# Kernel optimization log

Measured on AMD Instinct MI355X. Metric: run time of the kernel, lower is better.

The kernel has to match this reference:

```python
import jax, jax.numpy as jnp
import numpy as np

ALPHA = 0.5
EPS = 1e-6


def setup_inputs() -> dict:
    key = jax.random.key(0)
    k1, k2, k3 = jax.random.split(key, 3)
    B, N = 8192, 4096
    y_pred = jax.random.uniform(k1, (B, N), dtype=jnp.float32)
    y_true = jax.random.randint(k2, (B, N), 0, 2).astype(jnp.float32)
    depth_weights = jax.random.uniform(k3, (B, N), dtype=jnp.float32)
    return {"y_pred": y_pred, "y_true": y_true, "depth_weights": depth_weights}


def reference(y_pred, y_true, depth_weights):
    B, N = y_true.shape
    # --- weighted BCE ---
    bce = -(y_true * jnp.log(y_pred + EPS) + (1.0 - y_true) * jnp.log(1.0 - y_pred + EPS))
    wbce = jnp.mean(depth_weights * bce)

    # --- continuity-weighted loss: max run of correct predictions per row ---
    y_bin = (y_pred > 0.5).astype(y_true.dtype)
    correct = (y_bin == y_true)  # bool [B, N]
    idx = jnp.arange(N, dtype=jnp.int32)
    # position (1-based) of most recent incorrect element; 0 if none yet
    reset = jnp.where(correct, 0, idx + 1)  # [B, N]
    last_reset = jax.lax.cummax(reset, axis=1)  # [B, N]
    streak = (idx + 1)[None, :] - last_reset  # current run length at each position
    max_streak = jnp.max(streak, axis=1).astype(jnp.float32)  # [B]
    cwl = jnp.mean(1.0 - max_streak / N)

    return ALPHA * wbce + (1.0 - ALPHA) * cwl
```

## Files before the change

### kernel.cpp

```cpp
#include <hip/hip_runtime.h>

#define EPS 1e-6f

struct RunStats { int len, pre, suf, mx; };

__device__ inline RunStats rcombine(const RunStats& a, const RunStats& b) {
    RunStats r;
    r.len = a.len + b.len;
    r.pre = (a.pre == a.len) ? (a.len + b.pre) : a.pre;
    r.suf = (b.suf == b.len) ? (b.len + a.suf) : b.suf;
    r.mx  = max(max(a.mx, b.mx), a.suf + b.pre);
    return r;
}

__global__ __launch_bounds__(256) void row_kernel(
        const float* __restrict__ yp, const float* __restrict__ yt,
        const float* __restrict__ dw,
        float* __restrict__ row_wbce, int* __restrict__ row_streak) {
    const int row  = blockIdx.x;
    const int lane = threadIdx.x & 63;
    const int wave = threadIdx.x >> 6;
    const long base = (long)row * 4096;

    float sum = 0.0f;
    RunStats wstat = {0, 0, 0, 0};

    #pragma unroll
    for (int j = 0; j < 4; ++j) {
        const int e = wave * 1024 + j * 256 + lane * 4;
        const float4 p = *(const float4*)(yp + base + e);
        const float4 t = *(const float4*)(yt + base + e);
        const float4 w = *(const float4*)(dw + base + e);

        const float px[4] = {p.x, p.y, p.z, p.w};
        const float tx[4] = {t.x, t.y, t.z, t.w};
        const float wx[4] = {w.x, w.y, w.z, w.w};

        int bits = 0;
        #pragma unroll
        for (int c = 0; c < 4; ++c) {
            const float l1 = __logf(px[c] + EPS);
            const float l2 = __logf(1.0f - px[c] + EPS);
            const float bce = -(tx[c] * l1 + (1.0f - tx[c]) * l2);
            sum += wx[c] * bce;
            const bool pb = px[c] > 0.5f;
            const bool tb = tx[c] != 0.0f;
            bits |= (int)(pb == tb) << c;
        }

        int run = 0, m = 0;
        #pragma unroll
        for (int c = 0; c < 4; ++c) {
            run = ((bits >> c) & 1) ? run + 1 : 0;
            m = max(m, run);
        }
        const int pre = (bits & 1) ? ((bits & 2) ? ((bits & 4) ? ((bits & 8) ? 4 : 3) : 2) : 1) : 0;

        int packed = pre | (run << 10) | (m << 20);
        int alen = 4;
        #pragma unroll
        for (int off = 1; off < 64; off <<= 1) {
            const int o = __shfl_down(packed, off);
            const int apre = packed & 1023, asuf = (packed >> 10) & 1023, amx = packed >> 20;
            const int bpre = o & 1023,      bsuf = (o >> 10) & 1023,      bmx = o >> 20;
            const int npre = (apre == alen) ? (alen + bpre) : apre;
            const int nsuf = (bsuf == alen) ? (alen + asuf) : bsuf;
            const int nmx  = max(max(amx, bmx), asuf + bpre);
            packed = npre | (nsuf << 10) | (nmx << 20);
            alen <<= 1;
        }
        RunStats g;
        g.len = 256;
        g.pre = packed & 1023;
        g.suf = (packed >> 10) & 1023;
        g.mx  = packed >> 20;
        wstat = rcombine(wstat, g);
    }

    #pragma unroll
    for (int off = 32; off; off >>= 1) sum += __shfl_down(sum, off);

    __shared__ RunStats sstat[4];
    __shared__ float ssum[4];
    if (lane == 0) { sstat[wave] = wstat; ssum[wave] = sum; }
    __syncthreads();
    if (threadIdx.x == 0) {
        RunStats r = rcombine(rcombine(sstat[0], sstat[1]), rcombine(sstat[2], sstat[3]));
        row_wbce[row]   = ssum[0] + ssum[1] + ssum[2] + ssum[3];
        row_streak[row] = r.mx;
    }
}

__global__ __launch_bounds__(256) void finalize_kernel(
        const float* __restrict__ row_wbce, const int* __restrict__ row_streak,
        int rows, float* __restrict__ out) {
    double s = 0.0;
    long long st = 0;
    for (int i = threadIdx.x; i < rows; i += 256) {
        s  += (double)row_wbce[i];
        st += (long long)row_streak[i];
    }
    __shared__ double sd[256];
    __shared__ long long sl[256];
    sd[threadIdx.x] = s; sl[threadIdx.x] = st;
    __syncthreads();
    for (int o = 128; o; o >>= 1) {
        if (threadIdx.x < o) {
            sd[threadIdx.x] += sd[threadIdx.x + o];
            sl[threadIdx.x] += sl[threadIdx.x + o];
        }
        __syncthreads();
    }
    if (threadIdx.x == 0) {
        const double total = (double)rows * 4096.0;
        const double wbce = sd[0] / total;
        const double cwl  = 1.0 - (double)sl[0] / total;
        out[0] = (float)(0.5 * wbce + 0.5 * cwl);
    }
}

extern "C" void kernel_launch(void* const* d_in, const int* in_sizes, int n_in,
                              void* d_out, int out_size, void* d_ws, size_t ws_size,
                              hipStream_t stream) {
    const float* yp = (const float*)d_in[0];
    const float* yt = (const float*)d_in[1];
    const float* dw = (const float*)d_in[2];
    float* out = (float*)d_out;

    const int rows = in_sizes[0] / 4096;
    float* row_wbce  = (float*)d_ws;
    int*   row_streak = (int*)((char*)d_ws + (size_t)rows * sizeof(float));

    row_kernel<<<rows, 256, 0, stream>>>(yp, yt, dw, row_wbce, row_streak);
    finalize_kernel<<<1, 256, 0, stream>>>(row_wbce, row_streak, rows, out);
}
```

Before: 358.7 us.

## Give each thread 16 contiguous elements, use one log, bitmask run stats

Each thread now loads 16 contiguous elements (four float4 per input, all issued up front) instead of four strided float4 groups. BCE uses a single log per element by selecting p or 1-p from the binary label, with the negation moved to the end. Run statistics are computed from a 16-bit mask with ctz/clz and a shift-and loop, so only one cross-lane scan per wave is needed instead of four. The finalize kernel grows to 1024 threads. The single-log form assumes labels are exactly 0 or 1, and the denser load pattern may change coalescing.

Result: faster. 349.4 us (-2.6%).

```diff
diff --git a/kernel.cpp b/kernel.cpp
--- a/kernel.cpp
+++ b/kernel.cpp
@@ -20,91 +20,90 @@
     const int row  = blockIdx.x;
     const int lane = threadIdx.x & 63;
     const int wave = threadIdx.x >> 6;
-    const long base = (long)row * 4096;
+    const long base = (long)row * 4096 + wave * 1024 + lane * 16;
+
+    float4 p[4], t[4], w[4];
+    #pragma unroll
+    for (int q = 0; q < 4; ++q) {
+        p[q] = *(const float4*)(yp + base + q * 4);
+        t[q] = *(const float4*)(yt + base + q * 4);
+        w[q] = *(const float4*)(dw + base + q * 4);
+    }
 
     float sum = 0.0f;
-    RunStats wstat = {0, 0, 0, 0};
-
+    unsigned mask = 0;
     #pragma unroll
-    for (int j = 0; j < 4; ++j) {
-        const int e = wave * 1024 + j * 256 + lane * 4;
-        const float4 p = *(const float4*)(yp + base + e);
-        const float4 t = *(const float4*)(yt + base + e);
-        const float4 w = *(const float4*)(dw + base + e);
-
-        const float px[4] = {p.x, p.y, p.z, p.w};
-        const float tx[4] = {t.x, t.y, t.z, t.w};
-        const float wx[4] = {w.x, w.y, w.z, w.w};
-
-        int bits = 0;
+    for (int q = 0; q < 4; ++q) {
+        const float pp[4] = {p[q].x, p[q].y, p[q].z, p[q].w};
+        const float tt[4] = {t[q].x, t[q].y, t[q].z, t[q].w};
+        const float ww[4] = {w[q].x, w[q].y, w[q].z, w[q].w};
         #pragma unroll
         for (int c = 0; c < 4; ++c) {
-            const float l1 = __logf(px[c] + EPS);
-            const float l2 = __logf(1.0f - px[c] + EPS);
-            const float bce = -(tx[c] * l1 + (1.0f - tx[c]) * l2);
-            sum += wx[c] * bce;
-            const bool pb = px[c] > 0.5f;
-            const bool tb = tx[c] != 0.0f;
-            bits |= (int)(pb == tb) << c;
+            const bool tb = tt[c] != 0.0f;
+            const float v = (tb ? pp[c] : 1.0f - pp[c]) + EPS;
+            sum = fmaf(ww[c], __logf(v), sum);
+            const bool pb = pp[c] > 0.5f;
+            mask |= (unsigned)(pb == tb) << (q * 4 + c);
         }
+    }
 
-        int run = 0, m = 0;
-        #pragma unroll
-        for (int c = 0; c < 4; ++c) {
-            run = ((bits >> c) & 1) ? run + 1 : 0;
-            m = max(m, run);
-        }
-        const int pre = (bits & 1) ? ((bits & 2) ? ((bits & 4) ? ((bits & 8) ? 4 : 3) : 2) : 1) : 0;
-
-        int packed = pre | (run << 10) | (m << 20);
-        int alen = 4;
-        #pragma unroll
-        for (int off = 1; off < 64; off <<= 1) {
-            const int o = __shfl_down(packed, off);
-            const int apre = packed & 1023, asuf = (packed >> 10) & 1023, amx = packed >> 20;
-            const int bpre = o & 1023,      bsuf = (o >> 10) & 1023,      bmx = o >> 20;
-            const int npre = (apre == alen) ? (alen + bpre) : apre;
-            const int nsuf = (bsuf == alen) ? (alen + asuf) : bsuf;
-            const int nmx  = max(max(amx, bmx), asuf + bpre);
-            packed = npre | (nsuf << 10) | (nmx << 20);
-            alen <<= 1;
-        }
-        RunStats g;
-        g.len = 256;
-        g.pre = packed & 1023;
-        g.suf = (packed >> 10) & 1023;
-        g.mx  = packed >> 20;
-        wstat = rcombine(wstat, g);
-    }
+    int pre = __builtin_ctz(~mask);
+    int suf = __builtin_clz(~(mask << 16));
+    int mx = 0;
+    { unsigned x = mask; while (x) { x &= (x << 1); ++mx; } }
 
     #pragma unroll
     for (int off = 32; off; off >>= 1) sum += __shfl_down(sum, off);
 
+    int packed = pre | (suf << 10) | (mx << 20);
+    int alen = 16;
+    #pragma unroll
+    for (int off = 1; off < 32; off <<= 1) {
+        const int o = __shfl_down(packed, off);
+        const int apre = packed & 1023, asuf = (packed >> 10) & 1023, amx = packed >> 20;
+        const int bpre = o & 1023,      bsuf = (o >> 10) & 1023,      bmx = o >> 20;
+        const int npre = (apre == alen) ? (alen + bpre) : apre;
+        const int nsuf = (bsuf == alen) ? (alen + asuf) : bsuf;
+        const int nmx  = max(max(amx, bmx), asuf + bpre);
+        packed = npre | (nsuf << 10) | (nmx << 20);
+        alen <<= 1;
+    }
+    RunStats g;
+    {
+        const int o = __shfl_down(packed, 32);
+        const int apre = packed & 1023, asuf = (packed >> 10) & 1023, amx = packed >> 20;
+        const int bpre = o & 1023,      bsuf = (o >> 10) & 1023,      bmx = o >> 20;
+        g.len = 1024;
+        g.pre = (apre == 512) ? (512 + bpre) : apre;
+        g.suf = (bsuf == 512) ? (512 + asuf) : bsuf;
+        g.mx  = max(max(amx, bmx), asuf + bpre);
+    }
+
     __shared__ RunStats sstat[4];
     __shared__ float ssum[4];
-    if (lane == 0) { sstat[wave] = wstat; ssum[wave] = sum; }
+    if (lane == 0) { sstat[wave] = g; ssum[wave] = sum; }
     __syncthreads();
     if (threadIdx.x == 0) {
         RunStats r = rcombine(rcombine(sstat[0], sstat[1]), rcombine(sstat[2], sstat[3]));
-        row_wbce[row]   = ssum[0] + ssum[1] + ssum[2] + ssum[3];
+        row_wbce[row]   = -(ssum[0] + ssum[1] + ssum[2] + ssum[3]);
         row_streak[row] = r.mx;
     }
 }
 
-__global__ __launch_bounds__(256) void finalize_kernel(
+__global__ __launch_bounds__(1024) void finalize_kernel(
         const float* __restrict__ row_wbce, const int* __restrict__ row_streak,
         int rows, float* __restrict__ out) {
     double s = 0.0;
     long long st = 0;
-    for (int i = threadIdx.x; i < rows; i += 256) {
+    for (int i = threadIdx.x; i < rows; i += 1024) {
         s  += (double)row_wbce[i];
         st += (long long)row_streak[i];
     }
-    __shared__ double sd[256];
-    __shared__ long long sl[256];
+    __shared__ double sd[1024];
+    __shared__ long long sl[1024];
     sd[threadIdx.x] = s; sl[threadIdx.x] = st;
     __syncthreads();
-    for (int o = 128; o; o >>= 1) {
+    for (int o = 512; o; o >>= 1) {
         if (threadIdx.x < o) {
             sd[threadIdx.x] += sd[threadIdx.x + o];
             sl[threadIdx.x] += sl[threadIdx.x + o];
@@ -128,9 +127,9 @@
     float* out = (float*)d_out;
 
     const int rows = in_sizes[0] / 4096;
-    float* row_wbce  = (float*)d_ws;
+    float* row_wbce   = (float*)d_ws;
     int*   row_streak = (int*)((char*)d_ws + (size_t)rows * sizeof(float));
 
     row_kernel<<<rows, 256, 0, stream>>>(yp, yt, dw, row_wbce, row_streak);
-    finalize_kernel<<<1, 256, 0, stream>>>(row_wbce, row_streak, rows, out);
+    finalize_kernel<<<1, 1024, 0, stream>>>(row_wbce, row_streak, rows, out);
 }
```
